# Optimization experiments

Hardware: AMD Instinct MI355X
Metric: run time of the kernel (lower is better)

## Reference

```python
import jax, jax.numpy as jnp
import numpy as np
import math

B, N = 1, 512
C_S, C_Z, C_H, H, L, RECYCLE = 384, 128, 16, 12, 8, 2


def setup_inputs():
    key = jax.random.key(0)
    ks = jax.random.split(key, 16)
    w = lambda k, shape: jax.random.normal(k, shape, dtype=jnp.float32) * 0.02
    return {
        's': jax.random.normal(ks[0], (B, N, C_S), jnp.float32),
        'z': jax.random.normal(ks[1], (B, N, N, C_Z), jnp.float32),
        'Wq': w(ks[2], (L, C_S, H * C_H)), 'bq': jnp.zeros((L, H * C_H), jnp.float32),
        'Wk': w(ks[3], (L, C_S, H * C_H)), 'bk': jnp.zeros((L, H * C_H), jnp.float32),
        'Wv': w(ks[4], (L, C_S, H * C_H)), 'bv': jnp.zeros((L, H * C_H), jnp.float32),
        'Wb': w(ks[5], (L, C_Z, H)), 'bb': jnp.zeros((L, H), jnp.float32),
        'Wo': w(ks[6], (L, H * (C_H + C_Z), C_S)), 'bo': jnp.zeros((L, C_S), jnp.float32),
        'Wt1': w(ks[7], (L, C_S, 4 * C_S)), 'bt1': jnp.zeros((L, 4 * C_S), jnp.float32),
        'Wt2': w(ks[8], (L, 4 * C_S, C_S)), 'bt2': jnp.zeros((L, C_S), jnp.float32),
        'Wu': w(ks[9], (L, C_S, 6)), 'bu': jnp.zeros((L, 6), jnp.float32),
        'ln_g': jnp.ones((2 * L, C_S), jnp.float32),
        'ln_b': jnp.zeros((2 * L, C_S), jnp.float32),
    }


def _layer_norm(x, g, b, eps=1e-5):
    mu = jnp.mean(x, axis=-1, keepdims=True)
    var = jnp.mean((x - mu) ** 2, axis=-1, keepdims=True)
    return (x - mu) / jnp.sqrt(var + eps) * g + b


def _forward(s, z, Wq, bq, Wk, bk, Wv, bv, Wb, bb, Wo, bo, Wt1, bt1, Wt2, bt2, Wu, bu, ln_g, ln_b):
    b_, n_, _ = s.shape
    coords = jnp.zeros((b_, n_, 3), s.dtype)
    inv_sqrt_c = 1.0 / math.sqrt(C_H)
    for _r in range(RECYCLE):
        for i in range(L):
            # ---- Invariant Point Attention ----
            q = (s @ Wq[i] + bq[i]).reshape(b_, n_, H, C_H)
            k = (s @ Wk[i] + bk[i]).reshape(b_, n_, H, C_H)
            v = (s @ Wv[i] + bv[i]).reshape(b_, n_, H, C_H)
            attn = jnp.einsum('bihc,bjhc->bijh', q, k) * inv_sqrt_c  # (B,N,N,H)
            bias_z = z @ Wb[i] + bb[i]  # (B,N,N,H)
            # multiscale cdist bias: <=5A -> 1.0, <=15A -> 0.3, else 0.05
            sq = jnp.sum((coords[:, :, None, :] - coords[:, None, :, :]) ** 2, axis=-1)
            d = jnp.sqrt(jnp.maximum(sq, 1e-12))
            ms = jnp.where(d <= 5.0, 1.0, jnp.where(d <= 15.0, 0.3, 0.05))[..., None]
            attn = attn + bias_z + ms
            wgt = jax.nn.softmax(attn, axis=2)  # softmax over j
            scalar = jnp.einsum('bijh,bjhc->bihc', wgt, v)
            pair = jnp.einsum('bijh,bijc->bihc', wgt, z)
            o = jnp.concatenate([scalar, pair], axis=-1).reshape(b_, n_, H * (C_H + C_Z))
            s = _layer_norm(s + (o @ Wo[i] + bo[i]), ln_g[2 * i], ln_b[2 * i])
            # ---- Transition (FFN) ----
            t = jax.nn.relu(s @ Wt1[i] + bt1[i]) @ Wt2[i] + bt2[i]
            s = _layer_norm(s + t, ln_g[2 * i + 1], ln_b[2 * i + 1])
            # ---- Backbone update: source discards quaternion, applies translation only ----
            upd = s @ Wu[i] + bu[i]
            coords = coords + upd[..., :3]
    return coords


def reference(s, z, Wq, bq, Wk, bk, Wv, bv, Wb, bb, Wo, bo, Wt1, bt1, Wt2, bt2, Wu, bu, ln_g, ln_b):
    return _forward(s, z, Wq, bq, Wk, bk, Wv, bv, Wb, bb, Wo, bo, Wt1, bt1, Wt2, bt2, Wu, bu, ln_g, ln_b)
```

## Files before the change

kernel.cpp:

```cpp
#include <hip/hip_runtime.h>


constexpr int N    = 512;
constexpr int CS   = 384;
constexpr int CZ   = 128;
constexpr int CH   = 16;
constexpr int H    = 12;
constexpr int L    = 8;
constexpr int RECY = 2;
constexpr int HCH  = H * CH;
constexpr int QKVN = 3 * HCH;
constexpr int OD   = H * (CH + CZ);
constexpr int FF   = 4 * CS;
constexpr int MB   = 96;
constexpr long long NN2 = (long long)N * N;

typedef __bf16 bf16x8 __attribute__((ext_vector_type(8)));
typedef float  f32x4  __attribute__((ext_vector_type(4)));
typedef unsigned short us8 __attribute__((ext_vector_type(8)));

__device__ __forceinline__ ushort f2bf(float f) {
    uint u = __builtin_bit_cast(uint, f);
    return (ushort)((u + 0x7fffu + ((u >> 16) & 1u)) >> 16);
}
__device__ __forceinline__ float bf2f(ushort h) {
    uint u = ((uint)h) << 16;
    return __builtin_bit_cast(float, u);
}

__global__ __launch_bounds__(256) void init_s(
    const float* __restrict__ s_in, float* __restrict__ scur, ushort* __restrict__ sbf)
{
    int i = blockIdx.x * 256 + threadIdx.x;
    float v = s_in[i];
    scur[i] = v;
    sbf[i]  = f2bf(v);
}

__global__ __launch_bounds__(256) void pack_bqkv(
    const float* __restrict__ bq, const float* __restrict__ bk,
    const float* __restrict__ bv, float* __restrict__ bqkv)
{
    int idx = blockIdx.x * 256 + threadIdx.x;
    if (idx >= L * QKVN) return;
    int n = idx % QKVN, l = idx / QKVN;
    int sel = n / HCH, nn = n % HCH;
    const float* bp = sel == 0 ? bq : (sel == 1 ? bk : bv);
    bqkv[idx] = bp[l * HCH + nn];
}

__global__ __launch_bounds__(256) void pack_qkv_t(
    const float* __restrict__ Wq, const float* __restrict__ Wk,
    const float* __restrict__ Wv, ushort* __restrict__ WqkvT)
{
    __shared__ float tile[32][33];
    const int l = blockIdx.z;
    const int k0 = blockIdx.x * 32, n0 = blockIdx.y * 32;
    const int tx = threadIdx.x & 31, ty = threadIdx.x >> 5;
    const int sel = n0 / HCH;
    const int nn0 = n0 - sel * HCH;
    const float* W = sel == 0 ? Wq : (sel == 1 ? Wk : Wv);
    #pragma unroll
    for (int r = 0; r < 32; r += 8)
        tile[ty + r][tx] = W[((size_t)l * CS + k0 + ty + r) * HCH + nn0 + tx];
    __syncthreads();
    #pragma unroll
    for (int r = 0; r < 32; r += 8)
        WqkvT[((size_t)l * QKVN + n0 + ty + r) * CS + k0 + tx] = f2bf(tile[tx][ty + r]);
}

__global__ __launch_bounds__(256) void transpose_w(
    const float* __restrict__ in, ushort* __restrict__ out, int K, int Nn)
{
    __shared__ float tile[32][33];
    const int l = blockIdx.z;
    const float* ip = in + (size_t)l * K * Nn;
    ushort* op = out + (size_t)l * K * Nn;
    const int k0 = blockIdx.x * 32, n0 = blockIdx.y * 32;
    const int tx = threadIdx.x & 31, ty = threadIdx.x >> 5;
    #pragma unroll
    for (int r = 0; r < 32; r += 8)
        tile[ty + r][tx] = ip[(size_t)(k0 + ty + r) * Nn + n0 + tx];
    __syncthreads();
    #pragma unroll
    for (int r = 0; r < 32; r += 8)
        op[(size_t)(n0 + ty + r) * K + k0 + tx] = f2bf(tile[tx][ty + r]);
}

__global__ __launch_bounds__(256) void pack_wbt(
    const float* __restrict__ Wb, ushort* __restrict__ WbT)
{
    int idx = blockIdx.x * 256 + threadIdx.x;
    int m = idx >> 7, c = idx & 127;
    int l = m / H, h = m % H;
    WbT[idx] = f2bf(Wb[((size_t)l * CZ + c) * H + h]);
}

__global__ __launch_bounds__(256) void bias_gemm(
    const ushort* __restrict__ WbT, const float* __restrict__ z,
    const float* __restrict__ bb, ushort* __restrict__ bias_all)
{
    const int w = threadIdx.x >> 6, lane = threadIdx.x & 63;
    const int lm = lane & 15, kg = lane >> 4;
    const size_t ij0 = (size_t)blockIdx.x * 256 + (size_t)w * 64;
    __shared__ float bbs[MB];
    if (threadIdx.x < MB) bbs[threadIdx.x] = bb[threadIdx.x];
    __syncthreads();
    f32x4 acc[6][4];
    #pragma unroll
    for (int mt = 0; mt < 6; mt++)
        #pragma unroll
        for (int nt = 0; nt < 4; nt++) acc[mt][nt] = (f32x4){0.f, 0.f, 0.f, 0.f};
    #pragma unroll
    for (int kc = 0; kc < 4; kc++) {
        const int k = kc * 32 + kg * 8;
        bf16x8 b[4];
        #pragma unroll
        for (int nt = 0; nt < 4; nt++) {
            const float* zp = z + (ij0 + nt * 16 + lm) * CZ + k;
            float4 z0 = *(const float4*)zp, z1 = *(const float4*)(zp + 4);
            b[nt][0] = (__bf16)z0.x; b[nt][1] = (__bf16)z0.y;
            b[nt][2] = (__bf16)z0.z; b[nt][3] = (__bf16)z0.w;
            b[nt][4] = (__bf16)z1.x; b[nt][5] = (__bf16)z1.y;
            b[nt][6] = (__bf16)z1.z; b[nt][7] = (__bf16)z1.w;
        }
        #pragma unroll
        for (int mt = 0; mt < 6; mt++) {
            bf16x8 a = *(const bf16x8*)(WbT + (size_t)(mt * 16 + lm) * CZ + k);
            #pragma unroll
            for (int nt = 0; nt < 4; nt++)
                acc[mt][nt] = __builtin_amdgcn_mfma_f32_16x16x32_bf16(a, b[nt], acc[mt][nt], 0, 0, 0);
        }
    }
    #pragma unroll
    for (int mt = 0; mt < 6; mt++)
        #pragma unroll
        for (int nt = 0; nt < 4; nt++)
            #pragma unroll
            for (int r = 0; r < 4; r++) {
                int m = mt * 16 + kg * 4 + r;
                bias_all[(size_t)m * NN2 + ij0 + nt * 16 + lm] = f2bf(acc[mt][nt][r] + bbs[m]);
            }
}

__global__ __launch_bounds__(256) void gemm_bf16(
    const ushort* __restrict__ A, const ushort* __restrict__ Bt,
    const float* __restrict__ bias, float* __restrict__ C, ushort* __restrict__ Cbf,
    ushort* __restrict__ vTout,
    int M, int Nn, int K, int kper, int relu)
{
    const int w = threadIdx.x >> 6, lane = threadIdx.x & 63;
    const int lm = lane & 15, kg = lane >> 4;
    const int m0 = blockIdx.y * 64 + w * 16;
    const int n0 = blockIdx.x * 64;
    const int kbeg = blockIdx.z * kper;
    const int kh = kper >> 1;
    const ushort* Ap  = A  + (size_t)(m0 + lm) * K + kbeg + kg * 8;
    const ushort* Bp  = Bt + (size_t)(n0 + lm) * K + kbeg + kg * 8;
    f32x4 acc[4], ac2[4];
    #pragma unroll
    for (int ct = 0; ct < 4; ct++) {
        acc[ct] = (f32x4){0.f, 0.f, 0.f, 0.f};
        ac2[ct] = (f32x4){0.f, 0.f, 0.f, 0.f};
    }
    for (int k = 0; k < kh; k += 32) {
        bf16x8 a0 = *(const bf16x8*)(Ap + k);
        bf16x8 a1 = *(const bf16x8*)(Ap + kh + k);
        #pragma unroll
        for (int ct = 0; ct < 4; ct++) {
            bf16x8 b0 = *(const bf16x8*)(Bp + (size_t)ct * 16 * K + k);
            bf16x8 b1 = *(const bf16x8*)(Bp + (size_t)ct * 16 * K + kh + k);
            acc[ct] = __builtin_amdgcn_mfma_f32_16x16x32_bf16(a0, b0, acc[ct], 0, 0, 0);
            ac2[ct] = __builtin_amdgcn_mfma_f32_16x16x32_bf16(a1, b1, ac2[ct], 0, 0, 0);
        }
    }
    float* Cz = C ? C + (size_t)blockIdx.z * M * Nn : nullptr;
    #pragma unroll
    for (int ct = 0; ct < 4; ct++) {
        int col = n0 + ct * 16 + lm;
        float bs = bias ? bias[col] : 0.f;
        float vv[4];
        #pragma unroll
        for (int r = 0; r < 4; r++) {
            int row = m0 + kg * 4 + r;
            float v = acc[ct][r] + ac2[ct][r] + bs;
            if (relu) v = fmaxf(v, 0.f);
            vv[r] = v;
            if (Cz)  Cz[(size_t)row * Nn + col] = v;
            if (Cbf) Cbf[(size_t)row * Nn + col] = f2bf(v);
        }
        if (vTout && col >= 2 * HCH) {
            ushort4 o;
            o.x = f2bf(vv[0]); o.y = f2bf(vv[1]); o.z = f2bf(vv[2]); o.w = f2bf(vv[3]);
            *(ushort4*)(vTout + (size_t)(col - 2 * HCH) * N + m0 + kg * 4) = o;
        }
    }
}

__global__ __launch_bounds__(256) void attn_fused(
    const float* __restrict__ qkv, const ushort* __restrict__ bias_l,
    const float* __restrict__ coords, const ushort* __restrict__ z_t,
    const ushort* __restrict__ vT, ushort* __restrict__ obuf)
{
    const int i = blockIdx.x, t = threadIdx.x;
    const int w = t >> 6, lane = t & 63;
    const int lm = lane & 15, kg = lane >> 4;
    __shared__ float  qs[HCH];
    __shared__ float  cj[N * 3];
    __shared__ ushort wgt[16 * N];

    if (t < HCH) qs[t] = qkv[(size_t)i * QKVN + t] * 0.25f;
    #pragma unroll
    for (int e = 0; e < 6; e++) cj[e * 256 + t] = coords[e * 256 + t];
    __syncthreads();

    const float cix = cj[i * 3 + 0], ciy = cj[i * 3 + 1], ciz = cj[i * 3 + 2];
    const int j0 = lane * 8;
    const int slot_us = (lane >> 2) * 512 + (lane & 3) * 128;

    #pragma unroll
    for (int e = 0; e < 4; e++) {
        const int h = w + 4 * e;
        ushort* wp = wgt + slot_us + h * 8;
        if (e == 3) { us8 zz = {}; *(us8*)wp = zz; continue; }
        float lg[8];
        us8 bl = *(const us8*)(bias_l + (size_t)h * NN2 + (size_t)i * N + j0);
        #pragma unroll
        for (int jj = 0; jj < 8; jj++) {
            const int j = j0 + jj;
            const float4* kp = (const float4*)(qkv + (size_t)j * QKVN + HCH + h * CH);
            const float4* qp = (const float4*)(qs + h * CH);
            float d = 0.f;
            #pragma unroll
            for (int cq = 0; cq < 4; cq++) {
                float4 kv = kp[cq], qv = qp[cq];
                d += qv.x * kv.x + qv.y * kv.y + qv.z * kv.z + qv.w * kv.w;
            }
            float dx = cix - cj[j * 3 + 0];
            float dy = ciy - cj[j * 3 + 1];
            float dz = ciz - cj[j * 3 + 2];
            float d2 = dx * dx + dy * dy + dz * dz;
            float ms = d2 <= 25.f ? 1.f : (d2 <= 225.f ? 0.3f : 0.05f);
            lg[jj] = d + bf2f(bl[jj]) + ms;
        }
        float mx = lg[0];
        #pragma unroll
        for (int jj = 1; jj < 8; jj++) mx = fmaxf(mx, lg[jj]);
        #pragma unroll
        for (int off = 32; off > 0; off >>= 1) mx = fmaxf(mx, __shfl_xor(mx, off));
        float ex[8], sm = 0.f;
        #pragma unroll
        for (int jj = 0; jj < 8; jj++) { ex[jj] = __expf(lg[jj] - mx); sm += ex[jj]; }
        #pragma unroll
        for (int off = 32; off > 0; off >>= 1) sm += __shfl_xor(sm, off);
        const float inv = 1.f / sm;
        us8 wv;
        #pragma unroll
        for (int jj = 0; jj < 8; jj++) wv[jj] = f2bf(ex[jj] * inv);
        *(us8*)wp = wv;
    }
    __syncthreads();

    const ushort* Bz = z_t + (size_t)i * CZ * N;
    f32x4 ap[2], as_[3];
    ap[0] = ap[1] = (f32x4){0.f, 0.f, 0.f, 0.f};
    as_[0] = as_[1] = as_[2] = (f32x4){0.f, 0.f, 0.f, 0.f};
    const int cbase = w * 32;
    const int pbase = 3 * w * 16;
    #pragma unroll 2
    for (int kk = 0; kk < 16; kk++) {
        bf16x8 a = *(const bf16x8*)(wgt + kk * 512 + lane * 8);
        const int ko = kk * 32 + kg * 8;
        #pragma unroll
        for (int ntl = 0; ntl < 2; ntl++) {
            bf16x8 b = *(const bf16x8*)(Bz + (size_t)(cbase + ntl * 16 + lm) * N + ko);
            ap[ntl] = __builtin_amdgcn_mfma_f32_16x16x32_bf16(a, b, ap[ntl], 0, 0, 0);
        }
        #pragma unroll
        for (int si = 0; si < 3; si++) {
            bf16x8 b = *(const bf16x8*)(vT + (size_t)(pbase + si * 16 + lm) * N + ko);
            as_[si] = __builtin_amdgcn_mfma_f32_16x16x32_bf16(a, b, as_[si], 0, 0, 0);
        }
    }
    const size_t ob = (size_t)i * OD;
    if (kg < 3) {
        #pragma unroll
        for (int ntl = 0; ntl < 2; ntl++)
            #pragma unroll
            for (int r = 0; r < 4; r++) {
                int h = kg * 4 + r;
                obuf[ob + h * 144 + 16 + cbase + ntl * 16 + lm] = f2bf(ap[ntl][r]);
            }
    }
    #pragma unroll
    for (int si = 0; si < 3; si++) {
        int ht = 3 * w + si;
        if (kg == (ht >> 2)) obuf[ob + ht * 144 + lm] = f2bf(as_[si][ht & 3]);
    }
}

template<int PARTS>
__global__ __launch_bounds__(128) void ln_residual(
    const float* __restrict__ x, const float* __restrict__ gb,
    float* __restrict__ s, ushort* __restrict__ sbf,
    const float* __restrict__ g, const float* __restrict__ b,
    const float* __restrict__ Wu_l, const float* __restrict__ bu_l,
    float* __restrict__ coords)
{
    const int i = blockIdx.x, t = threadIdx.x;
    __shared__ float red[4];
    __shared__ float redc[2][3];
    float v[3];
    float sum = 0.f;
    #pragma unroll
    for (int e = 0; e < 3; e++) {
        int c = t + e * 128;
        float a = s[(size_t)i * CS + c] + gb[c];
        #pragma unroll
        for (int p = 0; p < PARTS; p++) a += x[(size_t)p * N * CS + (size_t)i * CS + c];
        v[e] = a; sum += a;
    }
    #pragma unroll
    for (int off = 32; off > 0; off >>= 1) sum += __shfl_down(sum, off);
    if ((t & 63) == 0) red[t >> 6] = sum;
    __syncthreads();
    float mu = (red[0] + red[1]) * (1.f / CS);
    float vs = 0.f;
    #pragma unroll
    for (int e = 0; e < 3; e++) { float d = v[e] - mu; vs += d * d; }
    #pragma unroll
    for (int off = 32; off > 0; off >>= 1) vs += __shfl_down(vs, off);
    if ((t & 63) == 0) red[2 + (t >> 6)] = vs;
    __syncthreads();
    float inv = rsqrtf((red[2] + red[3]) * (1.f / CS) + 1e-5f);
    float a0 = 0.f, a1 = 0.f, a2 = 0.f;
    #pragma unroll
    for (int e = 0; e < 3; e++) {
        int c = t + e * 128;
        float ov = (v[e] - mu) * inv * g[c] + b[c];
        s[(size_t)i * CS + c]   = ov;
        sbf[(size_t)i * CS + c] = f2bf(ov);
        if (Wu_l) {
            a0 += ov * Wu_l[c * 6 + 0];
            a1 += ov * Wu_l[c * 6 + 1];
            a2 += ov * Wu_l[c * 6 + 2];
        }
    }
    if (Wu_l) {
        #pragma unroll
        for (int off = 32; off > 0; off >>= 1) {
            a0 += __shfl_down(a0, off);
            a1 += __shfl_down(a1, off);
            a2 += __shfl_down(a2, off);
        }
        if ((t & 63) == 0) {
            redc[t >> 6][0] = a0; redc[t >> 6][1] = a1; redc[t >> 6][2] = a2;
        }
        __syncthreads();
        if (t == 0) {
            coords[i * 3 + 0] += redc[0][0] + redc[1][0] + bu_l[0];
            coords[i * 3 + 1] += redc[0][1] + redc[1][1] + bu_l[1];
            coords[i * 3 + 2] += redc[0][2] + redc[1][2] + bu_l[2];
        }
    }
}

extern "C" void kernel_launch(void* const* d_in, const int* in_sizes, int n_in,
                              void* d_out, int out_size, void* d_ws, size_t ws_size,
                              hipStream_t stream)
{
    const float* s_in = (const float*)d_in[0];
    const float* z    = (const float*)d_in[1];
    const float* Wq   = (const float*)d_in[2];
    const float* bq   = (const float*)d_in[3];
    const float* Wk   = (const float*)d_in[4];
    const float* bk   = (const float*)d_in[5];
    const float* Wv   = (const float*)d_in[6];
    const float* bv   = (const float*)d_in[7];
    const float* Wb   = (const float*)d_in[8];
    const float* bb   = (const float*)d_in[9];
    const float* Wo   = (const float*)d_in[10];
    const float* bo   = (const float*)d_in[11];
    const float* Wt1  = (const float*)d_in[12];
    const float* bt1  = (const float*)d_in[13];
    const float* Wt2  = (const float*)d_in[14];
    const float* bt2  = (const float*)d_in[15];
    const float* Wu   = (const float*)d_in[16];
    const float* bu   = (const float*)d_in[17];
    const float* lng  = (const float*)d_in[18];
    const float* lnb  = (const float*)d_in[19];
    float* coords = (float*)d_out;

    float* wsf   = (float*)d_ws;
    float* qkv   = wsf;
    float* tmp2  = qkv + (size_t)N * QKVN;
    float* scur  = tmp2 + (size_t)9 * N * CS;
    float* bqkv  = scur + (size_t)N * CS;
    ushort* wsu     = (ushort*)(bqkv + (size_t)L * QKVN);
    ushort* bias_all= wsu;
    ushort* z_t     = bias_all + (size_t)MB * NN2;
    ushort* WqkvT   = z_t + (size_t)N * CZ * N;
    ushort* WoT     = WqkvT + (size_t)L * CS * QKVN;
    ushort* Wt1T    = WoT + (size_t)L * OD * CS;
    ushort* Wt2T    = Wt1T + (size_t)L * CS * FF;
    ushort* WbT     = Wt2T + (size_t)L * FF * CS;
    ushort* vT      = WbT + (size_t)MB * CZ;
    ushort* scur_bf = vT + (size_t)HCH * N;
    ushort* obuf_bf = scur_bf + (size_t)N * CS;
    ushort* tmp1_bf = obuf_bf + (size_t)N * OD;
    (void)in_sizes; (void)n_in; (void)out_size; (void)ws_size;

    hipMemsetAsync(coords, 0, (size_t)N * 3 * sizeof(float), stream);
    init_s<<<(N * CS) / 256, 256, 0, stream>>>(s_in, scur, scur_bf);
    pack_bqkv<<<(L * QKVN + 255) / 256, 256, 0, stream>>>(bq, bk, bv, bqkv);
    pack_qkv_t<<<dim3(CS / 32, QKVN / 32, L), 256, 0, stream>>>(Wq, Wk, Wv, WqkvT);
    transpose_w<<<dim3(OD / 32, CS / 32, L), 256, 0, stream>>>(Wo, WoT, OD, CS);
    transpose_w<<<dim3(CS / 32, FF / 32, L), 256, 0, stream>>>(Wt1, Wt1T, CS, FF);
    transpose_w<<<dim3(FF / 32, CS / 32, L), 256, 0, stream>>>(Wt2, Wt2T, FF, CS);
    transpose_w<<<dim3(N / 32, CZ / 32, N), 256, 0, stream>>>(z, z_t, N, CZ);
    pack_wbt<<<(MB * CZ) / 256, 256, 0, stream>>>(Wb, WbT);
    bias_gemm<<<(int)(NN2 / 256), 256, 0, stream>>>(WbT, z, bb, bias_all);

    for (int r = 0; r < RECY; r++) {
        for (int l = 0; l < L; l++) {
            gemm_bf16<<<dim3(QKVN / 64, N / 64, 1), 256, 0, stream>>>(
                scur_bf, WqkvT + (size_t)l * CS * QKVN, bqkv + l * QKVN,
                qkv, nullptr, vT, N, QKVN, CS, CS, 0);
            attn_fused<<<N, 256, 0, stream>>>(
                qkv, bias_all + (size_t)l * H * NN2, coords, z_t, vT, obuf_bf);
            gemm_bf16<<<dim3(CS / 64, N / 64, 9), 256, 0, stream>>>(
                obuf_bf, WoT + (size_t)l * OD * CS, nullptr,
                tmp2, nullptr, nullptr, N, CS, OD, OD / 9, 0);
            ln_residual<9><<<N, 128, 0, stream>>>(
                tmp2, bo + l * CS, scur, scur_bf,
                lng + (size_t)(2 * l) * CS, lnb + (size_t)(2 * l) * CS,
                nullptr, nullptr, nullptr);
            gemm_bf16<<<dim3(FF / 64, N / 64, 1), 256, 0, stream>>>(
                scur_bf, Wt1T + (size_t)l * CS * FF, bt1 + l * FF,
                nullptr, tmp1_bf, nullptr, N, FF, CS, CS, 1);
            gemm_bf16<<<dim3(CS / 64, N / 64, 8), 256, 0, stream>>>(
                tmp1_bf, Wt2T + (size_t)l * FF * CS, nullptr,
                tmp2, nullptr, nullptr, N, CS, FF, FF / 8, 0);
            ln_residual<8><<<N, 128, 0, stream>>>(
                tmp2, bt2 + l * CS, scur, scur_bf,
                lng + (size_t)(2 * l + 1) * CS, lnb + (size_t)(2 * l + 1) * CS,
                Wu + (size_t)l * CS * 6, bu + l * 6, coords);
        }
    }
}
```

Before: 2.069 ms.

## Fuse per-layer kernel sequence into persistent megakernel with grid barriers

Replaces the 112 per-layer kernel launches with a single persistent kernel of 256 blocks that runs every recycle and layer stage and separates stages with a software grid barrier built on atomics. The goal is to remove launch gaps and tail idle time between the many small GEMM, attention and layernorm kernels. Split-K factors change to fit the fixed grid (3 for Wo, 4 for Wt2), and each block now handles two attention rows and two layernorm rows. Risks are lower parallelism in the attention and GEMM stages, spin-wait cost at each barrier, and deadlock if all 256 blocks cannot be resident at once.

After: 5.097 ms. 146% more time.

```diff
diff --git a/kernel.cpp b/kernel.cpp
--- a/kernel.cpp
+++ b/kernel.cpp
@@ -13,6 +13,7 @@
 constexpr int OD   = H * (CH + CZ);
 constexpr int FF   = 4 * CS;
 constexpr int MB   = 96;
+constexpr int NB   = 256;
 constexpr long long NN2 = (long long)N * N;
 
 typedef __bf16 bf16x8 __attribute__((ext_vector_type(8)));
@@ -26,6 +27,25 @@
 __device__ __forceinline__ float bf2f(ushort h) {
     uint u = ((uint)h) << 16;
     return __builtin_bit_cast(float, u);
+}
+
+__device__ __forceinline__ void gsync(uint* cnt, uint* gen)
+{
+    __syncthreads();
+    if (threadIdx.x == 0) {
+        __threadfence();
+        uint g = __hip_atomic_load(gen, __ATOMIC_RELAXED, __HIP_MEMORY_SCOPE_AGENT);
+        uint a = __hip_atomic_fetch_add(cnt, 1u, __ATOMIC_ACQ_REL, __HIP_MEMORY_SCOPE_AGENT);
+        if (a == NB - 1u) {
+            __hip_atomic_store(cnt, 0u, __ATOMIC_RELAXED, __HIP_MEMORY_SCOPE_AGENT);
+            __hip_atomic_store(gen, g + 1u, __ATOMIC_RELEASE, __HIP_MEMORY_SCOPE_AGENT);
+        } else {
+            while (__hip_atomic_load(gen, __ATOMIC_RELAXED, __HIP_MEMORY_SCOPE_AGENT) == g)
+                __builtin_amdgcn_s_sleep(1);
+        }
+        __threadfence();
+    }
+    __syncthreads();
 }
 
 __global__ __launch_bounds__(256) void init_s(
@@ -143,17 +163,18 @@
             }
 }
 
-__global__ __launch_bounds__(256) void gemm_bf16(
+__device__ __forceinline__ void gemm_tile(
     const ushort* __restrict__ A, const ushort* __restrict__ Bt,
-    const float* __restrict__ bias, float* __restrict__ C, ushort* __restrict__ Cbf,
-    ushort* __restrict__ vTout,
-    int M, int Nn, int K, int kper, int relu)
-{
-    const int w = threadIdx.x >> 6, lane = threadIdx.x & 63;
+    const float* __restrict__ bias, float* __restrict__ C,
+    ushort* __restrict__ Cbf, ushort* __restrict__ vTout,
+    int M, int Nn, int K, int kper, int relu,
+    int bx, int by, int bz, int t)
+{
+    const int w = t >> 6, lane = t & 63;
     const int lm = lane & 15, kg = lane >> 4;
-    const int m0 = blockIdx.y * 64 + w * 16;
-    const int n0 = blockIdx.x * 64;
-    const int kbeg = blockIdx.z * kper;
+    const int m0 = by * 64 + w * 16;
+    const int n0 = bx * 64;
+    const int kbeg = bz * kper;
     const int kh = kper >> 1;
     const ushort* Ap  = A  + (size_t)(m0 + lm) * K + kbeg + kg * 8;
     const ushort* Bp  = Bt + (size_t)(n0 + lm) * K + kbeg + kg * 8;
@@ -174,7 +195,7 @@
             ac2[ct] = __builtin_amdgcn_mfma_f32_16x16x32_bf16(a1, b1, ac2[ct], 0, 0, 0);
         }
     }
-    float* Cz = C ? C + (size_t)blockIdx.z * M * Nn : nullptr;
+    float* Cz = C ? C + (size_t)bz * M * Nn : nullptr;
     #pragma unroll
     for (int ct = 0; ct < 4; ct++) {
         int col = n0 + ct * 16 + lm;
@@ -197,21 +218,16 @@
     }
 }
 
-__global__ __launch_bounds__(256) void attn_fused(
-    const float* __restrict__ qkv, const ushort* __restrict__ bias_l,
-    const float* __restrict__ coords, const ushort* __restrict__ z_t,
-    const ushort* __restrict__ vT, ushort* __restrict__ obuf)
-{
-    const int i = blockIdx.x, t = threadIdx.x;
+__device__ __forceinline__ void attn_one(
+    int i, int t, const float* __restrict__ qkv, const ushort* __restrict__ bias_l,
+    const ushort* __restrict__ z_t, const ushort* __restrict__ vT,
+    ushort* __restrict__ obuf, float* qs, const float* cj, ushort* wgt)
+{
     const int w = t >> 6, lane = t & 63;
     const int lm = lane & 15, kg = lane >> 4;
-    __shared__ float  qs[HCH];
-    __shared__ float  cj[N * 3];
-    __shared__ ushort wgt[16 * N];
-
+
+    __syncthreads();
     if (t < HCH) qs[t] = qkv[(size_t)i * QKVN + t] * 0.25f;
-    #pragma unroll
-    for (int e = 0; e < 6; e++) cj[e * 256 + t] = coords[e * 256 + t];
     __syncthreads();
 
     const float cix = cj[i * 3 + 0], ciy = cj[i * 3 + 1], ciz = cj[i * 3 + 2];
@@ -299,22 +315,23 @@
     }
 }
 
-template<int PARTS>
-__global__ __launch_bounds__(128) void ln_residual(
+template<int PARTS, bool COORD>
+__device__ __forceinline__ void ln_rows2(
     const float* __restrict__ x, const float* __restrict__ gb,
     float* __restrict__ s, ushort* __restrict__ sbf,
     const float* __restrict__ g, const float* __restrict__ b,
     const float* __restrict__ Wu_l, const float* __restrict__ bu_l,
-    float* __restrict__ coords)
-{
-    const int i = blockIdx.x, t = threadIdx.x;
-    __shared__ float red[4];
-    __shared__ float redc[2][3];
+    float* __restrict__ coords, int i0, int t,
+    float* redA , float* redC )
+{
+    const int half = t >> 7, tt = t & 127;
+    const int i = i0 + half;
+    const int wih = (t >> 6) & 1;
     float v[3];
     float sum = 0.f;
     #pragma unroll
     for (int e = 0; e < 3; e++) {
-        int c = t + e * 128;
+        int c = tt + e * 128;
         float a = s[(size_t)i * CS + c] + gb[c];
         #pragma unroll
         for (int p = 0; p < PARTS; p++) a += x[(size_t)p * N * CS + (size_t)i * CS + c];
@@ -322,31 +339,31 @@
     }
     #pragma unroll
     for (int off = 32; off > 0; off >>= 1) sum += __shfl_down(sum, off);
-    if ((t & 63) == 0) red[t >> 6] = sum;
-    __syncthreads();
-    float mu = (red[0] + red[1]) * (1.f / CS);
+    if ((t & 63) == 0) redA[half * 4 + wih] = sum;
+    __syncthreads();
+    float mu = (redA[half * 4 + 0] + redA[half * 4 + 1]) * (1.f / CS);
     float vs = 0.f;
     #pragma unroll
     for (int e = 0; e < 3; e++) { float d = v[e] - mu; vs += d * d; }
     #pragma unroll
     for (int off = 32; off > 0; off >>= 1) vs += __shfl_down(vs, off);
-    if ((t & 63) == 0) red[2 + (t >> 6)] = vs;
-    __syncthreads();
-    float inv = rsqrtf((red[2] + red[3]) * (1.f / CS) + 1e-5f);
+    if ((t & 63) == 0) redA[half * 4 + 2 + wih] = vs;
+    __syncthreads();
+    float inv = rsqrtf((redA[half * 4 + 2] + redA[half * 4 + 3]) * (1.f / CS) + 1e-5f);
     float a0 = 0.f, a1 = 0.f, a2 = 0.f;
     #pragma unroll
     for (int e = 0; e < 3; e++) {
-        int c = t + e * 128;
+        int c = tt + e * 128;
         float ov = (v[e] - mu) * inv * g[c] + b[c];
         s[(size_t)i * CS + c]   = ov;
         sbf[(size_t)i * CS + c] = f2bf(ov);
-        if (Wu_l) {
+        if (COORD) {
             a0 += ov * Wu_l[c * 6 + 0];
             a1 += ov * Wu_l[c * 6 + 1];
             a2 += ov * Wu_l[c * 6 + 2];
         }
     }
-    if (Wu_l) {
+    if (COORD) {
         #pragma unroll
         for (int off = 32; off > 0; off >>= 1) {
             a0 += __shfl_down(a0, off);
@@ -354,14 +371,87 @@
             a2 += __shfl_down(a2, off);
         }
         if ((t & 63) == 0) {
-            redc[t >> 6][0] = a0; redc[t >> 6][1] = a1; redc[t >> 6][2] = a2;
+            float* rc = redC + (half * 2 + wih) * 3;
+            rc[0] = a0; rc[1] = a1; rc[2] = a2;
         }
         __syncthreads();
-        if (t == 0) {
-            coords[i * 3 + 0] += redc[0][0] + redc[1][0] + bu_l[0];
-            coords[i * 3 + 1] += redc[0][1] + redc[1][1] + bu_l[1];
-            coords[i * 3 + 2] += redc[0][2] + redc[1][2] + bu_l[2];
-        }
+        if (tt == 0) {
+            const float* rA = redC + (half * 2 + 0) * 3;
+            const float* rB = redC + (half * 2 + 1) * 3;
+            coords[i * 3 + 0] += rA[0] + rB[0] + bu_l[0];
+            coords[i * 3 + 1] += rA[1] + rB[1] + bu_l[1];
+            coords[i * 3 + 2] += rA[2] + rB[2] + bu_l[2];
+        }
+    }
+}
+
+struct MegaArgs {
+    const ushort* WqkvT; const float* bqkv;
+    const ushort* WoT;   const float* bo;
+    const ushort* Wt1T;  const float* bt1;
+    const ushort* Wt2T;  const float* bt2;
+    const float*  Wu;    const float* bu;
+    const float*  lng;   const float* lnb;
+    const ushort* bias_all; const ushort* z_t;
+    float* qkv; float* tmp2; float* scur;
+    ushort* vT; ushort* scur_bf; ushort* obuf_bf; ushort* tmp1_bf;
+    float* coords;
+    uint* bar_cnt; uint* bar_gen;
+};
+
+__global__ __launch_bounds__(256) void mega(MegaArgs a)
+{
+    const int bid = blockIdx.x;
+    const int t = threadIdx.x;
+    __shared__ float  qs[HCH];
+    __shared__ float  cj[N * 3];
+    __shared__ ushort wgt[16 * N];
+    __shared__ float  lnredA[8];
+    __shared__ float  lnredC[12];
+
+    for (int r = 0; r < RECY; r++)
+    for (int l = 0; l < L; l++) {
+        if (bid < 72)
+            gemm_tile(a.scur_bf, a.WqkvT + (size_t)l * CS * QKVN, a.bqkv + l * QKVN,
+                      a.qkv, nullptr, a.vT, N, QKVN, CS, CS, 0,
+                      bid % 9, bid / 9, 0, t);
+        gsync(a.bar_cnt, a.bar_gen);
+        {
+            #pragma unroll
+            for (int e = 0; e < 6; e++) cj[e * 256 + t] = a.coords[e * 256 + t];
+            const ushort* bias_l = a.bias_all + (size_t)l * H * NN2;
+            attn_one(bid,       t, a.qkv, bias_l, a.z_t, a.vT, a.obuf_bf, qs, cj, wgt);
+            attn_one(bid + 256, t, a.qkv, bias_l, a.z_t, a.vT, a.obuf_bf, qs, cj, wgt);
+        }
+        gsync(a.bar_cnt, a.bar_gen);
+        if (bid < 144) {
+            int bz = bid / 48, rem = bid % 48;
+            gemm_tile(a.obuf_bf, a.WoT + (size_t)l * OD * CS, nullptr,
+                      a.tmp2, nullptr, nullptr, N, CS, OD, 576, 0,
+                      rem % 6, rem / 6, bz, t);
+        }
+        gsync(a.bar_cnt, a.bar_gen);
+        ln_rows2<3, false>(a.tmp2, a.bo + l * CS, a.scur, a.scur_bf,
+                           a.lng + (size_t)(2 * l) * CS, a.lnb + (size_t)(2 * l) * CS,
+                           nullptr, nullptr, nullptr, bid * 2, t, lnredA, lnredC);
+        gsync(a.bar_cnt, a.bar_gen);
+        if (bid < 192)
+            gemm_tile(a.scur_bf, a.Wt1T + (size_t)l * CS * FF, a.bt1 + l * FF,
+                      nullptr, a.tmp1_bf, nullptr, N, FF, CS, CS, 1,
+                      bid % 24, bid / 24, 0, t);
+        gsync(a.bar_cnt, a.bar_gen);
+        if (bid < 192) {
+            int bz = bid / 48, rem = bid % 48;
+            gemm_tile(a.tmp1_bf, a.Wt2T + (size_t)l * FF * CS, nullptr,
+                      a.tmp2, nullptr, nullptr, N, CS, FF, 384, 0,
+                      rem % 6, rem / 6, bz, t);
+        }
+        gsync(a.bar_cnt, a.bar_gen);
+        ln_rows2<4, true>(a.tmp2, a.bt2 + l * CS, a.scur, a.scur_bf,
+                          a.lng + (size_t)(2 * l + 1) * CS, a.lnb + (size_t)(2 * l + 1) * CS,
+                          a.Wu + (size_t)l * CS * 6, a.bu + l * 6, a.coords,
+                          bid * 2, t, lnredA, lnredC);
+        gsync(a.bar_cnt, a.bar_gen);
     }
 }
 
@@ -408,9 +498,11 @@
     ushort* scur_bf = vT + (size_t)HCH * N;
     ushort* obuf_bf = scur_bf + (size_t)N * CS;
     ushort* tmp1_bf = obuf_bf + (size_t)N * OD;
+    uint*   bar     = (uint*)(tmp1_bf + (size_t)N * FF);
     (void)in_sizes; (void)n_in; (void)out_size; (void)ws_size;
 
     hipMemsetAsync(coords, 0, (size_t)N * 3 * sizeof(float), stream);
+    hipMemsetAsync(bar, 0, 2 * sizeof(uint), stream);
     init_s<<<(N * CS) / 256, 256, 0, stream>>>(s_in, scur, scur_bf);
     pack_bqkv<<<(L * QKVN + 255) / 256, 256, 0, stream>>>(bq, bk, bv, bqkv);
     pack_qkv_t<<<dim3(CS / 32, QKVN / 32, L), 256, 0, stream>>>(Wq, Wk, Wv, WqkvT);
@@ -421,30 +513,17 @@
     pack_wbt<<<(MB * CZ) / 256, 256, 0, stream>>>(Wb, WbT);
     bias_gemm<<<(int)(NN2 / 256), 256, 0, stream>>>(WbT, z, bb, bias_all);
 
-    for (int r = 0; r < RECY; r++) {
-        for (int l = 0; l < L; l++) {
-            gemm_bf16<<<dim3(QKVN / 64, N / 64, 1), 256, 0, stream>>>(
-                scur_bf, WqkvT + (size_t)l * CS * QKVN, bqkv + l * QKVN,
-                qkv, nullptr, vT, N, QKVN, CS, CS, 0);
-            attn_fused<<<N, 256, 0, stream>>>(
-                qkv, bias_all + (size_t)l * H * NN2, coords, z_t, vT, obuf_bf);
-            gemm_bf16<<<dim3(CS / 64, N / 64, 9), 256, 0, stream>>>(
-                obuf_bf, WoT + (size_t)l * OD * CS, nullptr,
-                tmp2, nullptr, nullptr, N, CS, OD, OD / 9, 0);
-            ln_residual<9><<<N, 128, 0, stream>>>(
-                tmp2, bo + l * CS, scur, scur_bf,
-                lng + (size_t)(2 * l) * CS, lnb + (size_t)(2 * l) * CS,
-                nullptr, nullptr, nullptr);
-            gemm_bf16<<<dim3(FF / 64, N / 64, 1), 256, 0, stream>>>(
-                scur_bf, Wt1T + (size_t)l * CS * FF, bt1 + l * FF,
-                nullptr, tmp1_bf, nullptr, N, FF, CS, CS, 1);
-            gemm_bf16<<<dim3(CS / 64, N / 64, 8), 256, 0, stream>>>(
-                tmp1_bf, Wt2T + (size_t)l * FF * CS, nullptr,
-                tmp2, nullptr, nullptr, N, CS, FF, FF / 8, 0);
-            ln_residual<8><<<N, 128, 0, stream>>>(
-                tmp2, bt2 + l * CS, scur, scur_bf,
-                lng + (size_t)(2 * l + 1) * CS, lnb + (size_t)(2 * l + 1) * CS,
-                Wu + (size_t)l * CS * 6, bu + l * 6, coords);
-        }
-    }
-}
+    MegaArgs ma;
+    ma.WqkvT = WqkvT; ma.bqkv = bqkv;
+    ma.WoT = WoT;     ma.bo = bo;
+    ma.Wt1T = Wt1T;   ma.bt1 = bt1;
+    ma.Wt2T = Wt2T;   ma.bt2 = bt2;
+    ma.Wu = Wu;       ma.bu = bu;
+    ma.lng = lng;     ma.lnb = lnb;
+    ma.bias_all = bias_all; ma.z_t = z_t;
+    ma.qkv = qkv; ma.tmp2 = tmp2; ma.scur = scur;
+    ma.vT = vT; ma.scur_bf = scur_bf; ma.obuf_bf = obuf_bf; ma.tmp1_bf = tmp1_bf;
+    ma.coords = coords;
+    ma.bar_cnt = bar; ma.bar_gen = bar + 1;
+    mega<<<NB, 256, 0, stream>>>(ma);
+}
```

## Fuse output projection, layernorms, FFN and coord update into one row-block kernel

Applied to the files above, without the earlier changes.

Replaces the split-K Wo GEMM, two layernorm kernels and two FFN GEMMs with one kernel that processes 16 rows per block. The attention output and the FFN hidden activations stay in swizzled LDS, and weights are streamed from global memory. This removes five launches per layer and the fp32 split-K partial buffers and their reduction traffic. The cost is only 32 blocks of 512 threads, so most CUs sit idle and each block rereads the full weight matrices.

Result: slower. 3.103 ms (+50.0%).

```diff
diff --git a/kernel.cpp b/kernel.cpp
--- a/kernel.cpp
+++ b/kernel.cpp
@@ -145,18 +145,16 @@
 
 __global__ __launch_bounds__(256) void gemm_bf16(
     const ushort* __restrict__ A, const ushort* __restrict__ Bt,
-    const float* __restrict__ bias, float* __restrict__ C, ushort* __restrict__ Cbf,
-    ushort* __restrict__ vTout,
-    int M, int Nn, int K, int kper, int relu)
+    const float* __restrict__ bias, float* __restrict__ C,
+    ushort* __restrict__ vTout, int M, int Nn, int K, int kper)
 {
     const int w = threadIdx.x >> 6, lane = threadIdx.x & 63;
     const int lm = lane & 15, kg = lane >> 4;
     const int m0 = blockIdx.y * 64 + w * 16;
     const int n0 = blockIdx.x * 64;
-    const int kbeg = blockIdx.z * kper;
     const int kh = kper >> 1;
-    const ushort* Ap  = A  + (size_t)(m0 + lm) * K + kbeg + kg * 8;
-    const ushort* Bp  = Bt + (size_t)(n0 + lm) * K + kbeg + kg * 8;
+    const ushort* Ap  = A  + (size_t)(m0 + lm) * K + kg * 8;
+    const ushort* Bp  = Bt + (size_t)(n0 + lm) * K + kg * 8;
     f32x4 acc[4], ac2[4];
     #pragma unroll
     for (int ct = 0; ct < 4; ct++) {
@@ -174,22 +172,19 @@
             ac2[ct] = __builtin_amdgcn_mfma_f32_16x16x32_bf16(a1, b1, ac2[ct], 0, 0, 0);
         }
     }
-    float* Cz = C ? C + (size_t)blockIdx.z * M * Nn : nullptr;
     #pragma unroll
     for (int ct = 0; ct < 4; ct++) {
         int col = n0 + ct * 16 + lm;
-        float bs = bias ? bias[col] : 0.f;
+        float bs = bias[col];
         float vv[4];
         #pragma unroll
         for (int r = 0; r < 4; r++) {
             int row = m0 + kg * 4 + r;
             float v = acc[ct][r] + ac2[ct][r] + bs;
-            if (relu) v = fmaxf(v, 0.f);
             vv[r] = v;
-            if (Cz)  Cz[(size_t)row * Nn + col] = v;
-            if (Cbf) Cbf[(size_t)row * Nn + col] = f2bf(v);
-        }
-        if (vTout && col >= 2 * HCH) {
+            C[(size_t)row * Nn + col] = v;
+        }
+        if (col >= 2 * HCH) {
             ushort4 o;
             o.x = f2bf(vv[0]); o.y = f2bf(vv[1]); o.z = f2bf(vv[2]); o.w = f2bf(vv[3]);
             *(ushort4*)(vTout + (size_t)(col - 2 * HCH) * N + m0 + kg * 4) = o;
@@ -299,68 +294,178 @@
     }
 }
 
-template<int PARTS>
-__global__ __launch_bounds__(128) void ln_residual(
-    const float* __restrict__ x, const float* __restrict__ gb,
-    float* __restrict__ s, ushort* __restrict__ sbf,
-    const float* __restrict__ g, const float* __restrict__ b,
+__global__ __launch_bounds__(512) void rowfused(
+    const ushort* __restrict__ obuf, const ushort* __restrict__ Wo_l,
+    const float* __restrict__ bo_l,
+    const ushort* __restrict__ Wt1_l, const float* __restrict__ bt1_l,
+    const ushort* __restrict__ Wt2_l, const float* __restrict__ bt2_l,
     const float* __restrict__ Wu_l, const float* __restrict__ bu_l,
+    const float* __restrict__ g1, const float* __restrict__ b1,
+    const float* __restrict__ g2, const float* __restrict__ b2,
+    float* __restrict__ scur, ushort* __restrict__ sbf_g,
     float* __restrict__ coords)
 {
-    const int i = blockIdx.x, t = threadIdx.x;
-    __shared__ float red[4];
-    __shared__ float redc[2][3];
-    float v[3];
-    float sum = 0.f;
-    #pragma unroll
-    for (int e = 0; e < 3; e++) {
-        int c = t + e * 128;
-        float a = s[(size_t)i * CS + c] + gb[c];
-        #pragma unroll
-        for (int p = 0; p < PARTS; p++) a += x[(size_t)p * N * CS + (size_t)i * CS + c];
-        v[e] = a; sum += a;
-    }
-    #pragma unroll
-    for (int off = 32; off > 0; off >>= 1) sum += __shfl_down(sum, off);
-    if ((t & 63) == 0) red[t >> 6] = sum;
-    __syncthreads();
-    float mu = (red[0] + red[1]) * (1.f / CS);
-    float vs = 0.f;
-    #pragma unroll
-    for (int e = 0; e < 3; e++) { float d = v[e] - mu; vs += d * d; }
-    #pragma unroll
-    for (int off = 32; off > 0; off >>= 1) vs += __shfl_down(vs, off);
-    if ((t & 63) == 0) red[2 + (t >> 6)] = vs;
-    __syncthreads();
-    float inv = rsqrtf((red[2] + red[3]) * (1.f / CS) + 1e-5f);
-    float a0 = 0.f, a1 = 0.f, a2 = 0.f;
-    #pragma unroll
-    for (int e = 0; e < 3; e++) {
-        int c = t + e * 128;
-        float ov = (v[e] - mu) * inv * g[c] + b[c];
-        s[(size_t)i * CS + c]   = ov;
-        sbf[(size_t)i * CS + c] = f2bf(ov);
-        if (Wu_l) {
-            a0 += ov * Wu_l[c * 6 + 0];
-            a1 += ov * Wu_l[c * 6 + 1];
-            a2 += ov * Wu_l[c * 6 + 2];
-        }
-    }
-    if (Wu_l) {
-        #pragma unroll
-        for (int off = 32; off > 0; off >>= 1) {
-            a0 += __shfl_down(a0, off);
-            a1 += __shfl_down(a1, off);
-            a2 += __shfl_down(a2, off);
-        }
-        if ((t & 63) == 0) {
-            redc[t >> 6][0] = a0; redc[t >> 6][1] = a1; redc[t >> 6][2] = a2;
-        }
-        __syncthreads();
-        if (t == 0) {
-            coords[i * 3 + 0] += redc[0][0] + redc[1][0] + bu_l[0];
-            coords[i * 3 + 1] += redc[0][1] + redc[1][1] + bu_l[1];
-            coords[i * 3 + 2] += redc[0][2] + redc[1][2] + bu_l[2];
+    constexpr int OBS = 1736;
+    constexpr int T1S = 1544;
+    constexpr int SAS = 388;
+    constexpr int SBS = 392;
+    __shared__ ushort obt1[16 * OBS];
+    __shared__ float  sar[16 * SAS];
+    __shared__ ushort sbf[16 * SBS];
+
+    const int t = threadIdx.x, w = t >> 6, lane = t & 63;
+    const int lm = lane & 15, kg = lane >> 4;
+    const int i0 = blockIdx.x * 16;
+    const int aswz = (lm & 3) << 3;
+
+    for (int v = t; v < 16 * (OD / 8); v += 512) {
+        int row = v / (OD / 8), c8 = (v % (OD / 8)) * 8;
+        *(us8*)&obt1[row * OBS + (c8 ^ ((row & 3) << 3))] =
+            *(const us8*)&obuf[(size_t)(i0 + row) * OD + c8];
+    }
+    __syncthreads();
+
+    f32x4 acc[12], ac2[3];
+
+    #pragma unroll
+    for (int ct = 0; ct < 3; ct++) {
+        acc[ct] = (f32x4){0.f, 0.f, 0.f, 0.f};
+        ac2[ct] = (f32x4){0.f, 0.f, 0.f, 0.f};
+    }
+    for (int k = 0; k < 864; k += 32) {
+        const int ka = kg * 8 + k;
+        bf16x8 a0 = *(const bf16x8*)&obt1[lm * OBS + (ka ^ aswz)];
+        bf16x8 a1 = *(const bf16x8*)&obt1[lm * OBS + ((ka + 864) ^ aswz)];
+        #pragma unroll
+        for (int ct = 0; ct < 3; ct++) {
+            const ushort* bp = Wo_l + (size_t)(w * 48 + ct * 16 + lm) * OD + ka;
+            acc[ct] = __builtin_amdgcn_mfma_f32_16x16x32_bf16(a0, *(const bf16x8*)bp, acc[ct], 0, 0, 0);
+            ac2[ct] = __builtin_amdgcn_mfma_f32_16x16x32_bf16(a1, *(const bf16x8*)(bp + 864), ac2[ct], 0, 0, 0);
+        }
+    }
+    #pragma unroll
+    for (int ct = 0; ct < 3; ct++) {
+        int col = w * 48 + ct * 16 + lm;
+        float bs = bo_l[col];
+        #pragma unroll
+        for (int rr = 0; rr < 4; rr++) {
+            int row = kg * 4 + rr;
+            sar[row * SAS + col] = acc[ct][rr] + ac2[ct][rr] + bs
+                                 + scur[(size_t)(i0 + row) * CS + col];
+        }
+    }
+    __syncthreads();
+
+    {
+        const int r = t >> 5, l32 = t & 31;
+        float vv[12], sum = 0.f;
+        #pragma unroll
+        for (int e = 0; e < 12; e++) { vv[e] = sar[r * SAS + l32 + e * 32]; sum += vv[e]; }
+        #pragma unroll
+        for (int off = 16; off > 0; off >>= 1) sum += __shfl_xor(sum, off);
+        float mu = sum * (1.f / CS);
+        float vs = 0.f;
+        #pragma unroll
+        for (int e = 0; e < 12; e++) { float d = vv[e] - mu; vs += d * d; }
+        #pragma unroll
+        for (int off = 16; off > 0; off >>= 1) vs += __shfl_xor(vs, off);
+        float inv = rsqrtf(vs * (1.f / CS) + 1e-5f);
+        #pragma unroll
+        for (int e = 0; e < 12; e++) {
+            int c = l32 + e * 32;
+            float o = (vv[e] - mu) * inv * g1[c] + b1[c];
+            sar[r * SAS + c] = o;
+            sbf[r * SBS + c] = f2bf(o);
+        }
+    }
+    __syncthreads();
+
+    #pragma unroll
+    for (int ct = 0; ct < 12; ct++) acc[ct] = (f32x4){0.f, 0.f, 0.f, 0.f};
+    for (int k = 0; k < 384; k += 32) {
+        bf16x8 a = *(const bf16x8*)&sbf[lm * SBS + kg * 8 + k];
+        #pragma unroll
+        for (int ct = 0; ct < 12; ct++) {
+            const ushort* bp = Wt1_l + (size_t)(w * 192 + ct * 16 + lm) * CS + kg * 8 + k;
+            acc[ct] = __builtin_amdgcn_mfma_f32_16x16x32_bf16(a, *(const bf16x8*)bp, acc[ct], 0, 0, 0);
+        }
+    }
+    #pragma unroll
+    for (int ct = 0; ct < 12; ct++) {
+        int col = w * 192 + ct * 16 + lm;
+        float bs = bt1_l[col];
+        #pragma unroll
+        for (int rr = 0; rr < 4; rr++) {
+            int row = kg * 4 + rr;
+            float v = fmaxf(acc[ct][rr] + bs, 0.f);
+            obt1[row * T1S + (((col & ~7) ^ ((row & 3) << 3)) | (col & 7))] = f2bf(v);
+        }
+    }
+    __syncthreads();
+
+    #pragma unroll
+    for (int ct = 0; ct < 3; ct++) {
+        acc[ct] = (f32x4){0.f, 0.f, 0.f, 0.f};
+        ac2[ct] = (f32x4){0.f, 0.f, 0.f, 0.f};
+    }
+    for (int k = 0; k < 768; k += 32) {
+        const int ka = kg * 8 + k;
+        bf16x8 a0 = *(const bf16x8*)&obt1[lm * T1S + (ka ^ aswz)];
+        bf16x8 a1 = *(const bf16x8*)&obt1[lm * T1S + ((ka + 768) ^ aswz)];
+        #pragma unroll
+        for (int ct = 0; ct < 3; ct++) {
+            const ushort* bp = Wt2_l + (size_t)(w * 48 + ct * 16 + lm) * FF + ka;
+            acc[ct] = __builtin_amdgcn_mfma_f32_16x16x32_bf16(a0, *(const bf16x8*)bp, acc[ct], 0, 0, 0);
+            ac2[ct] = __builtin_amdgcn_mfma_f32_16x16x32_bf16(a1, *(const bf16x8*)(bp + 768), ac2[ct], 0, 0, 0);
+        }
+    }
+    #pragma unroll
+    for (int ct = 0; ct < 3; ct++) {
+        int col = w * 48 + ct * 16 + lm;
+        float bs = bt2_l[col];
+        #pragma unroll
+        for (int rr = 0; rr < 4; rr++) {
+            int row = kg * 4 + rr;
+            sar[row * SAS + col] += acc[ct][rr] + ac2[ct][rr] + bs;
+        }
+    }
+    __syncthreads();
+
+    {
+        const int r = t >> 5, l32 = t & 31;
+        float vv[12], sum = 0.f;
+        #pragma unroll
+        for (int e = 0; e < 12; e++) { vv[e] = sar[r * SAS + l32 + e * 32]; sum += vv[e]; }
+        #pragma unroll
+        for (int off = 16; off > 0; off >>= 1) sum += __shfl_xor(sum, off);
+        float mu = sum * (1.f / CS);
+        float vs = 0.f;
+        #pragma unroll
+        for (int e = 0; e < 12; e++) { float d = vv[e] - mu; vs += d * d; }
+        #pragma unroll
+        for (int off = 16; off > 0; off >>= 1) vs += __shfl_xor(vs, off);
+        float inv = rsqrtf(vs * (1.f / CS) + 1e-5f);
+        float a0 = 0.f, a1 = 0.f, a2 = 0.f;
+        #pragma unroll
+        for (int e = 0; e < 12; e++) {
+            int c = l32 + e * 32;
+            float o = (vv[e] - mu) * inv * g2[c] + b2[c];
+            scur[(size_t)(i0 + r) * CS + c]  = o;
+            sbf_g[(size_t)(i0 + r) * CS + c] = f2bf(o);
+            a0 += o * Wu_l[c * 6 + 0];
+            a1 += o * Wu_l[c * 6 + 1];
+            a2 += o * Wu_l[c * 6 + 2];
+        }
+        #pragma unroll
+        for (int off = 16; off > 0; off >>= 1) {
+            a0 += __shfl_xor(a0, off);
+            a1 += __shfl_xor(a1, off);
+            a2 += __shfl_xor(a2, off);
+        }
+        if (l32 == 0) {
+            coords[(i0 + r) * 3 + 0] += a0 + bu_l[0];
+            coords[(i0 + r) * 3 + 1] += a1 + bu_l[1];
+            coords[(i0 + r) * 3 + 2] += a2 + bu_l[2];
         }
     }
 }
@@ -393,8 +498,7 @@
 
     float* wsf   = (float*)d_ws;
     float* qkv   = wsf;
-    float* tmp2  = qkv + (size_t)N * QKVN;
-    float* scur  = tmp2 + (size_t)9 * N * CS;
+    float* scur  = qkv + (size_t)N * QKVN;
     float* bqkv  = scur + (size_t)N * CS;
     ushort* wsu     = (ushort*)(bqkv + (size_t)L * QKVN);
     ushort* bias_all= wsu;
@@ -407,7 +511,6 @@
     ushort* vT      = WbT + (size_t)MB * CZ;
     ushort* scur_bf = vT + (size_t)HCH * N;
     ushort* obuf_bf = scur_bf + (size_t)N * CS;
-    ushort* tmp1_bf = obuf_bf + (size_t)N * OD;
     (void)in_sizes; (void)n_in; (void)out_size; (void)ws_size;
 
     hipMemsetAsync(coords, 0, (size_t)N * 3 * sizeof(float), stream);
@@ -425,26 +528,17 @@
         for (int l = 0; l < L; l++) {
             gemm_bf16<<<dim3(QKVN / 64, N / 64, 1), 256, 0, stream>>>(
                 scur_bf, WqkvT + (size_t)l * CS * QKVN, bqkv + l * QKVN,
-                qkv, nullptr, vT, N, QKVN, CS, CS, 0);
+                qkv, vT, N, QKVN, CS, CS);
             attn_fused<<<N, 256, 0, stream>>>(
                 qkv, bias_all + (size_t)l * H * NN2, coords, z_t, vT, obuf_bf);
-            gemm_bf16<<<dim3(CS / 64, N / 64, 9), 256, 0, stream>>>(
-                obuf_bf, WoT + (size_t)l * OD * CS, nullptr,
-                tmp2, nullptr, nullptr, N, CS, OD, OD / 9, 0);
-            ln_residual<9><<<N, 128, 0, stream>>>(
-                tmp2, bo + l * CS, scur, scur_bf,
+            rowfused<<<N / 16, 512, 0, stream>>>(
+                obuf_bf, WoT + (size_t)l * OD * CS, bo + l * CS,
+                Wt1T + (size_t)l * CS * FF, bt1 + l * FF,
+                Wt2T + (size_t)l * FF * CS, bt2 + l * CS,
+                Wu + (size_t)l * CS * 6, bu + l * 6,
                 lng + (size_t)(2 * l) * CS, lnb + (size_t)(2 * l) * CS,
-                nullptr, nullptr, nullptr);
-            gemm_bf16<<<dim3(FF / 64, N / 64, 1), 256, 0, stream>>>(
-                scur_bf, Wt1T + (size_t)l * CS * FF, bt1 + l * FF,
-                nullptr, tmp1_bf, nullptr, N, FF, CS, CS, 1);
-            gemm_bf16<<<dim3(CS / 64, N / 64, 8), 256, 0, stream>>>(
-                tmp1_bf, Wt2T + (size_t)l * FF * CS, nullptr,
-                tmp2, nullptr, nullptr, N, CS, FF, FF / 8, 0);
-            ln_residual<8><<<N, 128, 0, stream>>>(
-                tmp2, bt2 + l * CS, scur, scur_bf,
                 lng + (size_t)(2 * l + 1) * CS, lnb + (size_t)(2 * l + 1) * CS,
-                Wu + (size_t)l * CS * 6, bu + l * 6, coords);
-        }
-    }
-}
+                scur, scur_bf, coords);
+        }
+    }
+}
```
